# Kernel tuning notes

Hardware: AMD Instinct MI355X
Metric: run time of the kernel (lower is better)

## Reference

```python
import jax, jax.numpy as jnp
import numpy as np

NODES = 23   # 22 players + ball per frame-graph
K = 8        # random neighbors per node
B, T = 64, 128
G = B * T            # total graphs (frames)
N = G * NODES        # total nodes
D_IN, H, RH = 16, 128, 128


def setup_inputs() -> dict:
    key = jax.random.key(0)
    ks = jax.random.split(key, 10)
    x = jax.random.normal(ks[0], (N, D_IN), jnp.float32)
    # per-graph random edges: dst = each node repeated K times, src = random node in same graph
    src_local = jax.random.randint(ks[1], (G, NODES * K), 0, NODES)
    dst_local = jnp.tile(jnp.repeat(jnp.arange(NODES), K)[None, :], (G, 1))
    off = (jnp.arange(G) * NODES)[:, None]
    edge_index = jnp.stack([(src_local + off).reshape(-1),
                            (dst_local + off).reshape(-1)]).astype(jnp.int32)
    runner_idx = jax.random.randint(ks[2], (G,), 0, NODES, dtype=jnp.int32)
    sc = lambda k, sh: (jax.random.normal(k, sh, jnp.float32) * 0.05)
    return {
        'x': x, 'edge_index': edge_index, 'runner_idx': runner_idx,
        'W1': sc(ks[3], (D_IN, H)), 'b1': jnp.zeros((H,), jnp.float32),
        'W2': sc(ks[4], (H, H)),    'b2': jnp.zeros((H,), jnp.float32),
        'W_ih': sc(ks[5], (3 * RH, H)), 'W_hh': sc(ks[6], (3 * RH, RH)),
        'b_ih': jnp.zeros((3 * RH,), jnp.float32), 'b_hh': jnp.zeros((3 * RH,), jnp.float32),
        'Wp': sc(ks[7], (RH, 2)), 'bp': jnp.zeros((2,), jnp.float32),
    }


def _gcn_conv(h, edge_index, W, b):
    # PyG GCNConv: add self-loops, symmetric normalization, scatter-sum
    h = h @ W
    loop = jnp.arange(N, dtype=edge_index.dtype)
    s = jnp.concatenate([edge_index[0], loop])
    d = jnp.concatenate([edge_index[1], loop])
    deg = jax.ops.segment_sum(jnp.ones_like(s, h.dtype), d, num_segments=N)
    dinv = jnp.where(deg > 0, jax.lax.rsqrt(deg), 0.0)
    norm = dinv[s] * dinv[d]                      # [E+N]
    out = jax.ops.segment_sum(h[s] * norm[:, None], d, num_segments=N)
    return out + b


def _gru(seq, W_ih, W_hh, b_ih, b_hh):
    # torch GRU: gates in r,z,n order
    xg = seq @ W_ih.T + b_ih                      # [B,T,3RH]
    def step(hprev, xt):
        gh = hprev @ W_hh.T + b_hh
        xr, xz, xn = jnp.split(xt, 3, axis=-1)
        hr, hz, hn = jnp.split(gh, 3, axis=-1)
        r = jax.nn.sigmoid(xr + hr)
        z = jax.nn.sigmoid(xz + hz)
        n = jnp.tanh(xn + r * hn)
        hnew = (1.0 - z) * n + z * hprev
        return hnew, hnew
    h0 = jnp.zeros((seq.shape[0], RH), seq.dtype)
    _, outs = jax.lax.scan(step, h0, jnp.swapaxes(xg, 0, 1))
    return jnp.swapaxes(outs, 0, 1)               # [B,T,RH]


def reference(x, edge_index, runner_idx, W1, b1, W2, b2,
              W_ih, W_hh, b_ih, b_hh, Wp, bp):
    h = jax.nn.relu(_gcn_conv(x, edge_index, W1, b1))
    h = jax.nn.relu(_gcn_conv(h, edge_index, W2, b2))
    # fused equivalent of the per-graph nonzero()/indexing loop:
    runner_global = jnp.arange(G, dtype=jnp.int32) * NODES + runner_idx
    seq = h[runner_global].reshape(B, T, H)       # all lengths == T, padding is a no-op
    out = _gru(seq, W_ih, W_hh, b_ih, b_hh)
    return out @ Wp + bp                          # [B,T,2]
```

## Files before the change

kernel.cpp:

```cpp
#include <hip/hip_runtime.h>
#include <hip/hip_bf16.h>
#include <math.h>

#define GG 8192
#define NODESN 23
#define KK 8
#define DIN 16
#define HH 128
#define RHH 128
#define EPG (NODESN*KK)
#define TTT 128
#define BBB 64

typedef float v2f __attribute__((ext_vector_type(2)));

template<int CTRL>
static __device__ __forceinline__ float dpp_add(float v) {
    int x = __builtin_amdgcn_update_dpp(0, __float_as_int(v), CTRL, 0xF, 0xF, true);
    return v + __int_as_float(x);
}
#define DPP_XOR1 0xB1
#define DPP_XOR2 0x4E

__global__ __launch_bounds__(256) void gcn_hsum(
    const float* __restrict__ x, const int* __restrict__ esrc,
    const int* __restrict__ runner,
    const float* __restrict__ W1, const float* __restrict__ b1,
    float* __restrict__ xg)
{
    __shared__ float xs[NODESN * DIN];
    __shared__ int   srcs[EPG];
    __shared__ float t1[NODESN * HH];
    __shared__ float red[256];

    const int g   = blockIdx.x;
    const int tid = threadIdx.x;
    const int j   = tid & 127;
    const int nh  = tid >> 7;

    for (int i = tid; i < NODESN * DIN; i += 256) xs[i] = x[g * NODESN * DIN + i];
    for (int i = tid; i < EPG; i += 256)          srcs[i] = esrc[g * EPG + i] - g * NODESN;

    float w[DIN];
    #pragma unroll
    for (int k = 0; k < DIN; k++) w[k] = W1[k * HH + j];
    const float b1j = b1[j];
    __syncthreads();

    const int n0 = nh * 12;
    const int n1 = nh ? NODESN : 12;
    for (int n = n0; n < n1; n++) {
        float acc = 0.f;
        #pragma unroll
        for (int k = 0; k < DIN; k += 4) {
            float4 xv = *(const float4*)&xs[n * DIN + k];
            acc = fmaf(xv.x, w[k], fmaf(xv.y, w[k+1], fmaf(xv.z, w[k+2], fmaf(xv.w, w[k+3], acc))));
        }
        t1[n * HH + j] = acc;
    }
    __syncthreads();

    const int r = runner[g];
    float part = 0.f;
    for (int slot = nh; slot < 9; slot += 2) {
        int node = (slot < 8) ? srcs[r * KK + slot] : r;
        float acc = t1[node * HH + j];
        #pragma unroll
        for (int k = 0; k < KK; k++) acc += t1[srcs[node * KK + k] * HH + j];
        part += fmaxf(acc * (1.f / 9.f) + b1j, 0.f);
    }
    red[tid] = part;
    __syncthreads();
    if (tid < HH) xg[(size_t)g * 384 + tid] = red[tid] + red[tid + 128];
}

__global__ void pack_wih(const float* __restrict__ W, float* __restrict__ WTp)
{
    int idx = blockIdx.x * 256 + threadIdx.x;
    if (idx < 3 * RHH * RHH) {
        int j = idx / RHH, k = idx - j * RHH;
        WTp[(k >> 2) * (384 * 4) + j * 4 + (k & 3)] = W[idx];
    }
}

__global__ __launch_bounds__(384) void seqxg_kernel(
    float* __restrict__ xg, const float* __restrict__ W2,
    const float* __restrict__ b2, const float* __restrict__ WTp,
    const float* __restrict__ b_ih)
{
    __shared__ float hsb[16 * HH];
    __shared__ float sqb[16 * HH];
    const int tid = threadIdx.x;
    const size_t row0 = (size_t)blockIdx.x * 16;

    for (int v = tid; v < 16 * 32; v += 384) {
        int m = v >> 5, e = v & 31;
        ((float4*)hsb)[m * 32 + e] = *(const float4*)&xg[(row0 + m) * 384 + e * 4];
    }
    __syncthreads();

    {
        const int j = tid & 127, m0 = tid >> 7;
        const int nm = (m0 == 0) ? 6 : 5;
        float acc[6];
        #pragma unroll
        for (int t = 0; t < 6; t++) acc[t] = 0.f;
        for (int k = 0; k < HH; k += 4) {
            float w0 = W2[(k+0)*HH + j];
            float w1 = W2[(k+1)*HH + j];
            float w2 = W2[(k+2)*HH + j];
            float w3 = W2[(k+3)*HH + j];
            #pragma unroll
            for (int t = 0; t < 6; t++) {
                if (t < nm) {
                    float4 hv = *(const float4*)&hsb[(m0 + 3*t) * HH + k];
                    acc[t] = fmaf(hv.x, w0, fmaf(hv.y, w1, fmaf(hv.z, w2, fmaf(hv.w, w3, acc[t]))));
                }
            }
        }
        const float bj = b2[j];
        for (int t = 0; t < nm; t++)
            sqb[(m0 + 3*t) * HH + j] = fmaxf(acc[t] * (1.f/9.f) + bj, 0.f);
    }
    __syncthreads();

    {
        const int j2 = tid;
        float acc[16];
        const float bv = b_ih[j2];
        #pragma unroll
        for (int m = 0; m < 16; m++) acc[m] = bv;
        for (int k4 = 0; k4 < 32; k4++) {
            float4 wv = *(const float4*)&WTp[k4 * (384*4) + j2 * 4];
            #pragma unroll
            for (int m = 0; m < 16; m++) {
                float4 hv = *(const float4*)&sqb[m * HH + k4 * 4];
                acc[m] = fmaf(hv.x, wv.x, fmaf(hv.y, wv.y, fmaf(hv.z, wv.z, fmaf(hv.w, wv.w, acc[m]))));
            }
        }
        #pragma unroll
        for (int m = 0; m < 16; m++)
            xg[(row0 + m) * 384 + j2] = acc[m];
    }
}

#define CHUNK 32
#define NCH (TTT / CHUNK)
#define HPAD 132
#define XGB_FLOATS (CHUNK * HH * 4)

__global__ __launch_bounds__(512)
__attribute__((amdgpu_waves_per_eu(2, 2)))
void gru_kernel(
    const float* __restrict__ xg, const float* __restrict__ W_hh,
    const float* __restrict__ b_hh, const float* __restrict__ Wp,
    const float* __restrict__ bp, float* __restrict__ out)
{
    __shared__ float xgbuf[XGB_FLOATS];
    __shared__ float houtb[(CHUNK + 1) * HPAD];
    __shared__ float wps[2 * RHH + 2];

    const int b   = blockIdx.x;
    const int tid = threadIdx.x;
    const int q   = tid & 3;
    const int i   = tid >> 2;

    v2f wr2[16], wz2[16], wn2[16];
    int lof[8];
    {
        const float* br = W_hh + (size_t)i * RHH + q * 32;
        const float* bz = br + (size_t)RHH * RHH;
        const float* bn = bz + (size_t)RHH * RHH;
        #pragma unroll
        for (int m = 0; m < 8; m++) {
            int p = (m + 2 * q) & 7;
            lof[m] = q * 32 + 4 * p;
            float4 v;
            v = *(const float4*)(br + 4*p); wr2[2*m] = (v2f){v.x, v.y}; wr2[2*m+1] = (v2f){v.z, v.w};
            v = *(const float4*)(bz + 4*p); wz2[2*m] = (v2f){v.x, v.y}; wz2[2*m+1] = (v2f){v.z, v.w};
            v = *(const float4*)(bn + 4*p); wn2[2*m] = (v2f){v.x, v.y}; wn2[2*m+1] = (v2f){v.z, v.w};
        }
    }
    const float bhr = b_hh[i];
    const float bhz = b_hh[RHH + i];
    const float bhn = b_hh[2 * RHH + i];

    if (tid < 2 * RHH) wps[tid] = Wp[tid];
    if (tid < 2)       wps[2 * RHH + tid] = bp[tid];
    if (tid < HH)      houtb[tid] = 0.f;
    float hprev = 0.f;

    const float* xbase = xg + (size_t)b * TTT * 3 * RHH;
    float* outb = out + (size_t)b * TTT * 2;

    for (int c = 0; c < NCH; c++) {
        #pragma unroll
        for (int k2 = 0; k2 < 8; k2++) {
            int slot = tid + (k2 << 9);
            int tl = slot >> 7, ii = slot & 127;
            const float* gsrc = xbase + (size_t)(c * CHUNK + tl) * 384 + ii;
            float4 v;
            v.x = gsrc[0]; v.y = gsrc[128]; v.z = gsrc[256]; v.w = 0.f;
            *(float4*)&xgbuf[slot << 2] = v;
        }
        if (c > 0) {
            const int s  = tid & 3;
            const int cc = (tid >> 2) & 1;
            const int tl = tid >> 3;
            if (tl < CHUNK) {
                const float* hr = &houtb[(tl + 1) * HPAD + s * 32];
                float acc = 0.f;
                #pragma unroll
                for (int jj = 0; jj < 8; jj++) {
                    int mm = 4 * ((jj + 2 * s) & 7);
                    float4 hv = *(const float4*)(hr + mm);
                    int k = s * 32 + mm;
                    acc = fmaf(hv.x, wps[(k+0)*2 + cc],
                          fmaf(hv.y, wps[(k+1)*2 + cc],
                          fmaf(hv.z, wps[(k+2)*2 + cc],
                          fmaf(hv.w, wps[(k+3)*2 + cc], acc))));
                }
                acc = dpp_add<DPP_XOR1>(acc);
                acc = dpp_add<DPP_XOR2>(acc);
                if (s == 0)
                    outb[((c - 1) * CHUNK + tl) * 2 + cc] = acc + wps[2 * RHH + cc];
            }
        }
        __syncthreads();

        for (int tl = 0; tl < CHUNK; tl++) {
            const float* hrow = &houtb[tl * HPAD];
            float4 xgv = *(const float4*)&xgbuf[(tl * HH + i) << 2];
            v2f arA = (v2f){0.f, 0.f}, arB = arA, azA = arA, azB = arA, anA = arA, anB = arA;
            #pragma unroll
            for (int m = 0; m < 8; m++) {
                float4 hv = *(const float4*)(hrow + lof[m]);
                v2f h0 = (v2f){hv.x, hv.y};
                v2f h1 = (v2f){hv.z, hv.w};
                if (m & 1) {
                    arB = h0 * wr2[2*m] + arB; arB = h1 * wr2[2*m+1] + arB;
                    azB = h0 * wz2[2*m] + azB; azB = h1 * wz2[2*m+1] + azB;
                    anB = h0 * wn2[2*m] + anB; anB = h1 * wn2[2*m+1] + anB;
                } else {
                    arA = h0 * wr2[2*m] + arA; arA = h1 * wr2[2*m+1] + arA;
                    azA = h0 * wz2[2*m] + azA; azA = h1 * wz2[2*m+1] + azA;
                    anA = h0 * wn2[2*m] + anA; anA = h1 * wn2[2*m+1] + anA;
                }
            }
            v2f arv = arA + arB, azv = azA + azB, anv = anA + anB;
            float ar = arv.x + arv.y;
            float az = azv.x + azv.y;
            float an = anv.x + anv.y;

            ar = dpp_add<DPP_XOR1>(ar); ar = dpp_add<DPP_XOR2>(ar);
            az = dpp_add<DPP_XOR1>(az); az = dpp_add<DPP_XOR2>(az);
            an = dpp_add<DPP_XOR1>(an); an = dpp_add<DPP_XOR2>(an);

            {
                float sr = xgv.x + ar + bhr;
                float sz = xgv.y + az + bhz;
                float rg = 1.f / (1.f + __expf(-sr));
                float zg = 1.f / (1.f + __expf(-sz));
                float tv = fmaf(rg, an + bhn, xgv.z);
                tv = fminf(fmaxf(tv, -15.f), 15.f);
                float e2 = __expf(-2.f * tv);
                float ng = (1.f - e2) / (1.f + e2);
                hprev = fmaf(zg, hprev, (1.f - zg) * ng);
            }
            if (q == 0) houtb[(tl + 1) * HPAD + i] = hprev;
            __syncthreads();
        }
        if (q == 0) houtb[i] = hprev;
        __syncthreads();
    }

    {
        const int s  = tid & 3;
        const int cc = (tid >> 2) & 1;
        const int tl = tid >> 3;
        if (tl < CHUNK) {
            const float* hr = &houtb[(tl + 1) * HPAD + s * 32];
            float acc = 0.f;
            #pragma unroll
            for (int jj = 0; jj < 8; jj++) {
                int mm = 4 * ((jj + 2 * s) & 7);
                float4 hv = *(const float4*)(hr + mm);
                int k = s * 32 + mm;
                acc = fmaf(hv.x, wps[(k+0)*2 + cc],
                      fmaf(hv.y, wps[(k+1)*2 + cc],
                      fmaf(hv.z, wps[(k+2)*2 + cc],
                      fmaf(hv.w, wps[(k+3)*2 + cc], acc))));
            }
            acc = dpp_add<DPP_XOR1>(acc);
            acc = dpp_add<DPP_XOR2>(acc);
            if (s == 0)
                outb[((NCH - 1) * CHUNK + tl) * 2 + cc] = acc + wps[2 * RHH + cc];
        }
    }
}

extern "C" void kernel_launch(void* const* d_in, const int* in_sizes, int n_in,
                              void* d_out, int out_size, void* d_ws, size_t ws_size,
                              hipStream_t stream)
{
    const float* x      = (const float*)d_in[0];
    const int*   eidx   = (const int*)d_in[1];
    const int*   runner = (const int*)d_in[2];
    const float* W1     = (const float*)d_in[3];
    const float* b1     = (const float*)d_in[4];
    const float* W2     = (const float*)d_in[5];
    const float* b2     = (const float*)d_in[6];
    const float* W_ih   = (const float*)d_in[7];
    const float* W_hh   = (const float*)d_in[8];
    const float* b_ih   = (const float*)d_in[9];
    const float* b_hh   = (const float*)d_in[10];
    const float* Wp     = (const float*)d_in[11];
    const float* bp     = (const float*)d_in[12];
    float* out = (float*)d_out;

    float* xg  = (float*)d_ws;
    float* WTp = xg + (size_t)GG * 3 * RHH;

    pack_wih<<<192, 256, 0, stream>>>(W_ih, WTp);
    gcn_hsum<<<GG, 256, 0, stream>>>(x, eidx, runner, W1, b1, xg);
    seqxg_kernel<<<GG / 16, 384, 0, stream>>>(xg, W2, b2, WTp, b_ih);
    gru_kernel<<<BBB, 512, 0, stream>>>(xg, W_hh, b_hh, Wp, bp, out);
}
```

Baseline: 245.3 us.

## Compute two GRU hidden units per 8-lane group and prefetch next-step gate inputs

Changes the GRU recurrence mapping from 4 lanes per hidden unit to 8 lanes covering two hidden units, so each h vector load from shared memory feeds twice as many FMAs. The reduction becomes a 3-stage DPP (adding a half-row mirror) and the two results are written as a float2. It also prefetches the next timestep's xg gate values before the reduction to hide LDS latency. The cost is more per-thread gate math and an extra DPP stage on the serial critical path, with the same register budget for weights.

```diff
diff --git a/kernel.cpp b/kernel.cpp
--- a/kernel.cpp
+++ b/kernel.cpp
@@ -21,6 +21,7 @@
 }
 #define DPP_XOR1 0xB1
 #define DPP_XOR2 0x4E
+#define DPP_HMIR 0x141
 
 __global__ __launch_bounds__(256) void gcn_hsum(
     const float* __restrict__ x, const int* __restrict__ esrc,
@@ -162,33 +163,41 @@
 
     const int b   = blockIdx.x;
     const int tid = threadIdx.x;
-    const int q   = tid & 3;
-    const int i   = tid >> 2;
-
-    v2f wr2[16], wz2[16], wn2[16];
-    int lof[8];
+    const int q   = tid & 7;
+    const int u   = tid >> 3;
+
+    const int i0 = 2 * u, i1 = 2 * u + 1;
+
+    v2f wr0[8], wz0[8], wn0[8], wr1[8], wz1[8], wn1[8];
+    int lof[4];
     {
-        const float* br = W_hh + (size_t)i * RHH + q * 32;
-        const float* bz = br + (size_t)RHH * RHH;
-        const float* bn = bz + (size_t)RHH * RHH;
-        #pragma unroll
-        for (int m = 0; m < 8; m++) {
-            int p = (m + 2 * q) & 7;
-            lof[m] = q * 32 + 4 * p;
+        const float* r0 = W_hh + (size_t)i0 * RHH;
+        const float* z0 = r0 + (size_t)RHH * RHH;
+        const float* n0 = z0 + (size_t)RHH * RHH;
+        const float* r1 = W_hh + (size_t)i1 * RHH;
+        const float* z1 = r1 + (size_t)RHH * RHH;
+        const float* n1 = z1 + (size_t)RHH * RHH;
+        #pragma unroll
+        for (int m = 0; m < 4; m++) {
+            int p = (m + (q >> 1)) & 3;
+            int o = q * 16 + 4 * p;
+            lof[m] = o;
             float4 v;
-            v = *(const float4*)(br + 4*p); wr2[2*m] = (v2f){v.x, v.y}; wr2[2*m+1] = (v2f){v.z, v.w};
-            v = *(const float4*)(bz + 4*p); wz2[2*m] = (v2f){v.x, v.y}; wz2[2*m+1] = (v2f){v.z, v.w};
-            v = *(const float4*)(bn + 4*p); wn2[2*m] = (v2f){v.x, v.y}; wn2[2*m+1] = (v2f){v.z, v.w};
-        }
-    }
-    const float bhr = b_hh[i];
-    const float bhz = b_hh[RHH + i];
-    const float bhn = b_hh[2 * RHH + i];
+            v = *(const float4*)(r0 + o); wr0[2*m] = (v2f){v.x,v.y}; wr0[2*m+1] = (v2f){v.z,v.w};
+            v = *(const float4*)(z0 + o); wz0[2*m] = (v2f){v.x,v.y}; wz0[2*m+1] = (v2f){v.z,v.w};
+            v = *(const float4*)(n0 + o); wn0[2*m] = (v2f){v.x,v.y}; wn0[2*m+1] = (v2f){v.z,v.w};
+            v = *(const float4*)(r1 + o); wr1[2*m] = (v2f){v.x,v.y}; wr1[2*m+1] = (v2f){v.z,v.w};
+            v = *(const float4*)(z1 + o); wz1[2*m] = (v2f){v.x,v.y}; wz1[2*m+1] = (v2f){v.z,v.w};
+            v = *(const float4*)(n1 + o); wn1[2*m] = (v2f){v.x,v.y}; wn1[2*m+1] = (v2f){v.z,v.w};
+        }
+    }
+    const float bhr0 = b_hh[i0], bhz0 = b_hh[RHH + i0], bhn0 = b_hh[2 * RHH + i0];
+    const float bhr1 = b_hh[i1], bhz1 = b_hh[RHH + i1], bhn1 = b_hh[2 * RHH + i1];
 
     if (tid < 2 * RHH) wps[tid] = Wp[tid];
     if (tid < 2)       wps[2 * RHH + tid] = bp[tid];
     if (tid < HH)      houtb[tid] = 0.f;
-    float hprev = 0.f;
+    float hp0 = 0.f, hp1 = 0.f;
 
     const float* xbase = xg + (size_t)b * TTT * 3 * RHH;
     float* outb = out + (size_t)b * TTT * 2;
@@ -228,49 +237,74 @@
         }
         __syncthreads();
 
+        float4 x0 = *(const float4*)&xgbuf[(0 * HH + i0) << 2];
+        float4 x1 = *(const float4*)&xgbuf[(0 * HH + i1) << 2];
+
         for (int tl = 0; tl < CHUNK; tl++) {
             const float* hrow = &houtb[tl * HPAD];
-            float4 xgv = *(const float4*)&xgbuf[(tl * HH + i) << 2];
-            v2f arA = (v2f){0.f, 0.f}, arB = arA, azA = arA, azB = arA, anA = arA, anB = arA;
+            v2f ar0v = (v2f){0.f,0.f}, az0v = ar0v, an0v = ar0v;
+            v2f ar1v = ar0v, az1v = ar0v, an1v = ar0v;
             #pragma unroll
-            for (int m = 0; m < 8; m++) {
+            for (int m = 0; m < 4; m++) {
                 float4 hv = *(const float4*)(hrow + lof[m]);
                 v2f h0 = (v2f){hv.x, hv.y};
                 v2f h1 = (v2f){hv.z, hv.w};
-                if (m & 1) {
-                    arB = h0 * wr2[2*m] + arB; arB = h1 * wr2[2*m+1] + arB;
-                    azB = h0 * wz2[2*m] + azB; azB = h1 * wz2[2*m+1] + azB;
-                    anB = h0 * wn2[2*m] + anB; anB = h1 * wn2[2*m+1] + anB;
-                } else {
-                    arA = h0 * wr2[2*m] + arA; arA = h1 * wr2[2*m+1] + arA;
-                    azA = h0 * wz2[2*m] + azA; azA = h1 * wz2[2*m+1] + azA;
-                    anA = h0 * wn2[2*m] + anA; anA = h1 * wn2[2*m+1] + anA;
-                }
-            }
-            v2f arv = arA + arB, azv = azA + azB, anv = anA + anB;
-            float ar = arv.x + arv.y;
-            float az = azv.x + azv.y;
-            float an = anv.x + anv.y;
-
-            ar = dpp_add<DPP_XOR1>(ar); ar = dpp_add<DPP_XOR2>(ar);
-            az = dpp_add<DPP_XOR1>(az); az = dpp_add<DPP_XOR2>(az);
-            an = dpp_add<DPP_XOR1>(an); an = dpp_add<DPP_XOR2>(an);
+                ar0v = h0 * wr0[2*m] + ar0v; ar0v = h1 * wr0[2*m+1] + ar0v;
+                az0v = h0 * wz0[2*m] + az0v; az0v = h1 * wz0[2*m+1] + az0v;
+                an0v = h0 * wn0[2*m] + an0v; an0v = h1 * wn0[2*m+1] + an0v;
+                ar1v = h0 * wr1[2*m] + ar1v; ar1v = h1 * wr1[2*m+1] + ar1v;
+                az1v = h0 * wz1[2*m] + az1v; az1v = h1 * wz1[2*m+1] + az1v;
+                an1v = h0 * wn1[2*m] + an1v; an1v = h1 * wn1[2*m+1] + an1v;
+            }
+            float ar0 = ar0v.x + ar0v.y, az0 = az0v.x + az0v.y, an0 = an0v.x + an0v.y;
+            float ar1 = ar1v.x + ar1v.y, az1 = az1v.x + az1v.y, an1 = an1v.x + an1v.y;
+
+            float4 nx0, nx1;
+            if (tl + 1 < CHUNK) {
+                nx0 = *(const float4*)&xgbuf[((tl + 1) * HH + i0) << 2];
+                nx1 = *(const float4*)&xgbuf[((tl + 1) * HH + i1) << 2];
+            }
+
+            ar0 = dpp_add<DPP_XOR1>(ar0); ar0 = dpp_add<DPP_XOR2>(ar0); ar0 = dpp_add<DPP_HMIR>(ar0);
+            az0 = dpp_add<DPP_XOR1>(az0); az0 = dpp_add<DPP_XOR2>(az0); az0 = dpp_add<DPP_HMIR>(az0);
+            an0 = dpp_add<DPP_XOR1>(an0); an0 = dpp_add<DPP_XOR2>(an0); an0 = dpp_add<DPP_HMIR>(an0);
+            ar1 = dpp_add<DPP_XOR1>(ar1); ar1 = dpp_add<DPP_XOR2>(ar1); ar1 = dpp_add<DPP_HMIR>(ar1);
+            az1 = dpp_add<DPP_XOR1>(az1); az1 = dpp_add<DPP_XOR2>(az1); az1 = dpp_add<DPP_HMIR>(az1);
+            an1 = dpp_add<DPP_XOR1>(an1); an1 = dpp_add<DPP_XOR2>(an1); an1 = dpp_add<DPP_HMIR>(an1);
 
             {
-                float sr = xgv.x + ar + bhr;
-                float sz = xgv.y + az + bhz;
+                float sr = x0.x + ar0 + bhr0;
+                float sz = x0.y + az0 + bhz0;
                 float rg = 1.f / (1.f + __expf(-sr));
                 float zg = 1.f / (1.f + __expf(-sz));
-                float tv = fmaf(rg, an + bhn, xgv.z);
+                float tv = fmaf(rg, an0 + bhn0, x0.z);
                 tv = fminf(fmaxf(tv, -15.f), 15.f);
                 float e2 = __expf(-2.f * tv);
                 float ng = (1.f - e2) / (1.f + e2);
-                hprev = fmaf(zg, hprev, (1.f - zg) * ng);
-            }
-            if (q == 0) houtb[(tl + 1) * HPAD + i] = hprev;
+                hp0 = fmaf(zg, hp0, (1.f - zg) * ng);
+            }
+            {
+                float sr = x1.x + ar1 + bhr1;
+                float sz = x1.y + az1 + bhz1;
+                float rg = 1.f / (1.f + __expf(-sr));
+                float zg = 1.f / (1.f + __expf(-sz));
+                float tv = fmaf(rg, an1 + bhn1, x1.z);
+                tv = fminf(fmaxf(tv, -15.f), 15.f);
+                float e2 = __expf(-2.f * tv);
+                float ng = (1.f - e2) / (1.f + e2);
+                hp1 = fmaf(zg, hp1, (1.f - zg) * ng);
+            }
+            if (q == 0) {
+                float2 hw; hw.x = hp0; hw.y = hp1;
+                *(float2*)&houtb[(tl + 1) * HPAD + i0] = hw;
+            }
+            x0 = nx0; x1 = nx1;
             __syncthreads();
         }
-        if (q == 0) houtb[i] = hprev;
+        if (q == 0) {
+            float2 hw; hw.x = hp0; hw.y = hp1;
+            *(float2*)&houtb[i0] = hw;
+        }
         __syncthreads();
     }
 
```

After: 263.6 us. 1.07x slower.
